# Performance work log

Hardware: AMD Instinct MI355X
Metric: run time of the kernel (lower is better)

The kernel has to match this reference:

```python
import jax, jax.numpy as jnp
import numpy as np

N, E = 20000, 640000
F_IN, H, T = 64, 256, 64  # in_channels = T, edge_attr dim = T -> EdgeConv MLP in = 3*T


def _lin(key, fan_in, fan_out):
    k1, k2 = jax.random.split(key)
    s = 1.0 / np.sqrt(fan_in)
    W = jax.random.uniform(k1, (fan_in, fan_out), jnp.float32, -s, s)
    b = jax.random.uniform(k2, (fan_out,), jnp.float32, -s, s)
    return W, b


def setup_inputs() -> dict:
    key = jax.random.key(0)
    ks = jax.random.split(key, 12)
    x = jax.random.normal(ks[0], (N, F_IN), jnp.float32)
    edge_index = jax.random.randint(ks[1], (2, E), 0, N, jnp.int32)
    edge_attr = jax.random.normal(ks[2], (E, T), jnp.float32)
    conv1_W, conv1_b = _lin(ks[3], F_IN, H)
    e_W1, e_b1 = _lin(ks[4], 3 * T, H)
    e_W2, e_b2 = _lin(ks[5], H, H)
    conv2_W, conv2_b = _lin(ks[6], 2 * H, H)
    conv3_W, conv3_b = _lin(ks[7], H, F_IN)
    lin1_W, lin1_b = _lin(ks[8], 2 * F_IN, F_IN)
    lin2_W, lin2_b = _lin(ks[9], F_IN, 128)
    lin3_W, lin3_b = _lin(ks[10], 128, 32)
    lin4_W, lin4_b = _lin(ks[11], 32, 2)
    return dict(x=x, edge_index=edge_index, edge_attr=edge_attr,
                conv1_W=conv1_W, conv1_b=conv1_b,
                e_W1=e_W1, e_b1=e_b1, e_W2=e_W2, e_b2=e_b2,
                conv2_W=conv2_W, conv2_b=conv2_b,
                conv3_W=conv3_W, conv3_b=conv3_b,
                lin1_W=lin1_W, lin1_b=lin1_b, lin2_W=lin2_W, lin2_b=lin2_b,
                lin3_W=lin3_W, lin3_b=lin3_b, lin4_W=lin4_W, lin4_b=lin4_b)


def reference(x, edge_index, edge_attr,
              conv1_W, conv1_b, e_W1, e_b1, e_W2, e_b2,
              conv2_W, conv2_b, conv3_W, conv3_b,
              lin1_W, lin1_b, lin2_W, lin2_b, lin3_W, lin3_b, lin4_W, lin4_b):
    n = x.shape[0]
    src, dst = edge_index[0], edge_index[1]
    # GCN symmetric norm with self-loops (deg counted on dst, +1 for self-loop)
    deg = jax.ops.segment_sum(jnp.ones_like(src, jnp.float32), dst, num_segments=n) + 1.0
    dis = jax.lax.rsqrt(deg)

    def gcn(h, W, b):
        hw = h @ W
        msg = hw[src] * (dis[src] * dis[dst])[:, None]
        # self-loop contribution: norm = dis[i]^2
        return jax.ops.segment_sum(msg, dst, num_segments=n) + hw * (dis * dis)[:, None] + b

    out1 = jax.nn.relu(gcn(x, conv1_W, conv1_b))
    # EdgeConv: MLP(cat[x_i, x_j, edge_attr]) with max aggregation onto dst (x_i = target)
    m = jnp.concatenate([x[dst], x[src], edge_attr], axis=1)      # [E, 3T]
    m = jax.nn.relu(m @ e_W1 + e_b1) @ e_W2 + e_b2                 # [E, H]
    agg = jax.ops.segment_max(m, dst, num_segments=n)
    agg = jnp.where(jnp.isfinite(agg), agg, 0.0)                   # nodes with no in-edges
    out_e1 = jax.nn.relu(agg)

    out2 = jax.nn.relu(gcn(jnp.concatenate([out1, out_e1], axis=1), conv2_W, conv2_b))
    out3 = jax.nn.relu(gcn(out2, conv3_W, conv3_b))
    h = jnp.concatenate([x, out3], axis=1)
    h = jax.nn.softplus(h @ lin1_W + lin1_b)
    h = jax.nn.softplus(h @ lin2_W + lin2_b)
    h = jax.nn.softplus(h @ lin3_W + lin3_b)
    h = h @ lin4_W + lin4_b                                        # [N, 2]
    return (h[:, 0], h[:, 1])
```

## Files before the change

### kernel.cpp

```cpp
#include <hip/hip_runtime.h>
#include <stdint.h>

typedef __bf16 bf16x8 __attribute__((ext_vector_type(8)));
typedef float f32x4 __attribute__((ext_vector_type(4)));
typedef unsigned short u16x8 __attribute__((ext_vector_type(8)));
typedef unsigned long long ull_t;
typedef unsigned short ushort_t;

#define DEV __device__ __forceinline__

DEV unsigned short f2bf(float f) {
  __bf16 b = (__bf16)f;
  return __builtin_bit_cast(unsigned short, b);
}

DEV float bf2f(unsigned short b) { return __uint_as_float((unsigned int)b << 16); }

DEV f32x4 zero4() { f32x4 z = {0.f, 0.f, 0.f, 0.f}; return z; }

DEV float softplusf(float v) { return (v > 15.f) ? v : log1pf(expf(v)); }

__global__ void pack_weight(const float* __restrict__ W, unsigned short* __restrict__ P,
                            int K, int Ncols) {
  int idx = blockIdx.x * 256 + threadIdx.x;
  if (idx >= K * Ncols) return;
  int j = idx & 7;
  int lane = (idx >> 3) & 63;
  int rest = idx >> 9;
  int NT = Ncols >> 4;
  int nt = rest % NT;
  int kt = rest / NT;
  int k = kt * 32 + ((j >> 2) * 16) + ((lane >> 4) * 4) + (j & 3);
  int col = nt * 16 + (lane & 15);
  P[idx] = f2bf(W[(size_t)k * Ncols + col]);
}

__global__ void k_deg(const int* __restrict__ dst, int* __restrict__ degi, int E) {
  int i = blockIdx.x * 256 + threadIdx.x;
  if (i < E) atomicAdd(&degi[dst[i]], 1);
}

__global__ void k_dis(const int* __restrict__ degi, float* __restrict__ dis, int n) {
  int i = blockIdx.x * 256 + threadIdx.x;
  if (i < n) dis[i] = rsqrtf((float)degi[i] + 1.0f);
}

__global__ __launch_bounds__(1024) void k_scan(const int* __restrict__ degi,
                                               int* __restrict__ ptr, int n) {
  __shared__ int part[1024];
  const int tid = threadIdx.x;
  const int chunk = (n + 1023) / 1024;
  const int b = tid * chunk;
  const int e2 = min(n, b + chunk);
  int s = 0;
  for (int i = b; i < e2; ++i) s += degi[i];
  part[tid] = s;
  __syncthreads();
  for (int off = 1; off < 1024; off <<= 1) {
    int val = (tid >= off) ? part[tid - off] : 0;
    __syncthreads();
    part[tid] += val;
    __syncthreads();
  }
  int run = (tid == 0) ? 0 : part[tid - 1];
  for (int i = b; i < e2; ++i) {
    ptr[i] = run;
    run += degi[i];
  }
  if (tid == 1023) ptr[n] = run;
}

__global__ void k_fill(const int* __restrict__ srcs, const int* __restrict__ dsts,
                       const int* __restrict__ ptr, const float* __restrict__ dis,
                       int* __restrict__ fillc,
                       int2* __restrict__ sc_s, int* __restrict__ dst_s,
                       int* __restrict__ perm_s, int E) {
  int e = blockIdx.x * 256 + threadIdx.x;
  if (e >= E) return;
  int d = dsts[e];
  int s = srcs[e];
  int pos = ptr[d] + atomicAdd(&fillc[d], 1);
  float c = dis[s] * dis[d];
  sc_s[pos] = make_int2(s, __float_as_int(c));
  dst_s[pos] = d;
  perm_s[pos] = e;
}

template <int COLS, bool FINALIZE, bool INBF16>
__global__ __launch_bounds__(256) void k_gather_agg(
    const void* __restrict__ featv, const int2* __restrict__ sc,
    const int* __restrict__ ptr, const float* __restrict__ dis,
    const void* __restrict__ hwv, const float* __restrict__ bias,
    float* __restrict__ out, int n) {
  constexpr int V = COLS / 64;
  const int v = blockIdx.x * 4 + (threadIdx.x >> 6);
  if (v >= n) return;
  const int lane = threadIdx.x & 63;
  const int beg = ptr[v], end = ptr[v + 1];

  auto loadrow = [&](int s, float* f) {
    if constexpr (INBF16) {
      const ushort_t* feat = (const ushort_t*)featv;
      if constexpr (V == 4) {
        ushort4 u = *(const ushort4*)(feat + (size_t)s * COLS + lane * 4);
        f[0] = bf2f(u.x); f[1] = bf2f(u.y); f[2] = bf2f(u.z); f[3] = bf2f(u.w);
      } else {
        f[0] = bf2f(feat[(size_t)s * COLS + lane]);
      }
    } else {
      const float* feat = (const float*)featv;
      if constexpr (V == 4) {
        float4 q = *(const float4*)(feat + (size_t)s * COLS + lane * 4);
        f[0] = q.x; f[1] = q.y; f[2] = q.z; f[3] = q.w;
      } else {
        f[0] = feat[(size_t)s * COLS + lane];
      }
    }
  };

  float acc[V];
#pragma unroll
  for (int i = 0; i < V; ++i) acc[i] = 0.f;
  const int cnt = end - beg;
  const int2* scp = sc + beg;
  int i = 0;
  for (; i + 4 <= cnt; i += 4) {
    int2 s0 = scp[i], s1 = scp[i + 1], s2 = scp[i + 2], s3 = scp[i + 3];
    float f0[V], f1[V], f2[V], f3[V];
    loadrow(s0.x, f0); loadrow(s1.x, f1); loadrow(s2.x, f2); loadrow(s3.x, f3);
    float c0 = __int_as_float(s0.y), c1 = __int_as_float(s1.y);
    float c2 = __int_as_float(s2.y), c3 = __int_as_float(s3.y);
#pragma unroll
    for (int j = 0; j < V; ++j)
      acc[j] += f0[j] * c0 + f1[j] * c1 + f2[j] * c2 + f3[j] * c3;
  }
  for (; i < cnt; ++i) {
    int2 s0 = scp[i];
    float c0 = __int_as_float(s0.y);
    float f0[V];
    loadrow(s0.x, f0);
#pragma unroll
    for (int j = 0; j < V; ++j) acc[j] += f0[j] * c0;
  }
  float* op = out + (size_t)v * COLS + lane * V;
  if constexpr (FINALIZE) {
    const float dv = dis[v];
    float d2 = dv * dv;
    float h[V];
    if constexpr (INBF16) {
      const ushort_t* hw = (const ushort_t*)hwv;
      if constexpr (V == 4) {
        ushort4 u = *(const ushort4*)(hw + (size_t)v * COLS + lane * 4);
        h[0] = bf2f(u.x); h[1] = bf2f(u.y); h[2] = bf2f(u.z); h[3] = bf2f(u.w);
      } else {
        h[0] = bf2f(hw[(size_t)v * COLS + lane]);
      }
    } else {
      const float* hw = (const float*)hwv;
      if constexpr (V == 4) {
        float4 q = *(const float4*)(hw + (size_t)v * COLS + lane * 4);
        h[0] = q.x; h[1] = q.y; h[2] = q.z; h[3] = q.w;
      } else {
        h[0] = hw[(size_t)v * COLS + lane];
      }
    }
#pragma unroll
    for (int i2 = 0; i2 < V; ++i2)
      acc[i2] = fmaxf(acc[i2] + h[i2] * d2 + bias[lane * V + i2], 0.f);
  }
  if constexpr (V == 4) {
    *(float4*)op = make_float4(acc[0], acc[1], acc[2], acc[3]);
  } else {
    op[0] = acc[0];
  }
}

template <int K, int NOUT, bool COMPOSE, bool RELUBIAS, bool OUTBF16>
__global__ __launch_bounds__(256, 2) void gcn_gemm(
    const float* __restrict__ inA, const float* __restrict__ inB,
    const float* __restrict__ dis,
    const unsigned short* __restrict__ Wp, const float* __restrict__ bias,
    void* __restrict__ outv, int out_stride, int nrows) {
  constexpr int NT = NOUT / 16;
  constexpr int NTW = NOUT / 64;
  __shared__ unsigned short s_in[64 * K];
  const int tid = threadIdx.x;
  const int r0 = blockIdx.x * 64;

  constexpr int C4R = K / 4;
  for (int idx = tid; idx < 64 * C4R; idx += 256) {
    int row = idx / C4R;
    int rem = idx - row * C4R;
    int grow = r0 + row;
    float4 v = make_float4(0.f, 0.f, 0.f, 0.f);
    if (grow < nrows) {
      v = *(const float4*)&inA[(size_t)grow * K + rem * 4];
      if constexpr (COMPOSE) {
        float d = dis[grow];
        d *= d;
        float4 w2 = *(const float4*)&inB[(size_t)grow * K + rem * 4];
        v.x += w2.x * d; v.y += w2.y * d; v.z += w2.z * d; v.w += w2.w * d;
      }
    }
    ushort4 b;
    b.x = f2bf(v.x); b.y = f2bf(v.y); b.z = f2bf(v.z); b.w = f2bf(v.w);
    *(ushort4*)&s_in[row * K + ((rem ^ (row & 7)) * 4)] = b;
  }
  __syncthreads();

  const int lane = tid & 63, wid = tid >> 6;
  const int lr = lane & 15, lg = lane >> 4;
  f32x4 acc[4][NTW];
#pragma unroll
  for (int m = 0; m < 4; ++m)
#pragma unroll
    for (int n2 = 0; n2 < NTW; ++n2) acc[m][n2] = zero4();

#pragma unroll
  for (int kt = 0; kt < K / 32; ++kt) {
    bf16x8 a[4];
#pragma unroll
    for (int m = 0; m < 4; ++m) {
      int rA = m * 16 + lr;
      int c1 = (kt * 8 + lg) ^ (rA & 7);
      int c2 = (kt * 8 + lg + 4) ^ (rA & 7);
      union { bf16x8 v; ull_t q[2]; } u;
      u.q[0] = *(const ull_t*)&s_in[rA * K + c1 * 4];
      u.q[1] = *(const ull_t*)&s_in[rA * K + c2 * 4];
      a[m] = u.v;
    }
#pragma unroll
    for (int n2 = 0; n2 < NTW; ++n2) {
      int nt = wid * NTW + n2;
      bf16x8 b = *(const bf16x8*)&Wp[(((kt * NT + nt) * 64 + lane) * 8)];
#pragma unroll
      for (int m = 0; m < 4; ++m)
        acc[m][n2] = __builtin_amdgcn_mfma_f32_16x16x32_bf16(a[m], b, acc[m][n2], 0, 0, 0);
    }
  }

#pragma unroll
  for (int n2 = 0; n2 < NTW; ++n2) {
    int col = (wid * NTW + n2) * 16 + lr;
    float bv = 0.f;
    if (RELUBIAS) bv = bias[col];
#pragma unroll
    for (int m = 0; m < 4; ++m) {
#pragma unroll
      for (int r = 0; r < 4; ++r) {
        int grow = r0 + m * 16 + lg * 4 + r;
        if (grow < nrows) {
          float v = acc[m][n2][r];
          if (RELUBIAS) v = fmaxf(v + bv, 0.f);
          if constexpr (OUTBF16) {
            ((ushort_t*)outv)[(size_t)grow * out_stride + col] = f2bf(v);
          } else {
            ((float*)outv)[(size_t)grow * out_stride + col] = v;
          }
        }
      }
    }
  }
}

__global__ __launch_bounds__(512, 4) void k_edgeconv(
    const float* __restrict__ x, const float* __restrict__ ea,
    const int2* __restrict__ sc_s, const int* __restrict__ dst_s,
    const int* __restrict__ perm_s,
    const unsigned short* __restrict__ W1p, const float* __restrict__ b1,
    const unsigned short* __restrict__ W2p, const float* __restrict__ b2,
    float* __restrict__ h2, int E) {
  __shared__ unsigned short s_buf[256 * 72];
  __shared__ int s_src[64], s_dst[64], s_perm[64];
  __shared__ ull_t s_mask;
  const int tid = threadIdx.x;
  const int e0 = blockIdx.x * 64;
  const int lane = tid & 63, wid = tid >> 6;
  if (tid < 64) {
    int e = e0 + tid;
    s_src[tid] = (e < E) ? sc_s[e].x : 0;
    s_dst[tid] = (e < E) ? dst_s[e] : 0;
    s_perm[tid] = (e < E) ? perm_s[e] : 0;
  }
  __syncthreads();
  if (wid == 0) {
    bool chg = (lane > 0) && (s_dst[lane] != s_dst[lane - 1]);
    ull_t m = __ballot(chg);
    if (lane == 0) s_mask = m;
  }
#pragma unroll
  for (int seg = 0; seg < 3; ++seg) {
#pragma unroll
    for (int it = 0; it < 2; ++it) {
      int idx = it * 512 + tid;
      int ei = idx >> 4;
      int q = idx & 15;
      const float* row;
      if (seg == 0) row = x + (unsigned)s_dst[ei] * 64u;
      else if (seg == 1) row = x + (unsigned)s_src[ei] * 64u;
      else row = ea + (unsigned)s_perm[ei] * 64u;
      float4 v = make_float4(0.f, 0.f, 0.f, 0.f);
      if (e0 + ei < E) v = *(const float4*)(row + q * 4);
      ushort4 b;
      b.x = f2bf(v.x); b.y = f2bf(v.y); b.z = f2bf(v.z); b.w = f2bf(v.w);
      int chunk = (seg * 16 + q) ^ (ei & 7);
      *(ushort4*)&s_buf[ei * 192 + chunk * 4] = b;
    }
  }
  __syncthreads();

  const int wr = wid >> 2;
  const int wc = wid & 3;
  const int lr = lane & 15, lg = lane >> 4;
  f32x4 acc[2][4];
#pragma unroll
  for (int m = 0; m < 2; ++m)
#pragma unroll
    for (int n2 = 0; n2 < 4; ++n2) acc[m][n2] = zero4();

#pragma unroll
  for (int kt = 0; kt < 6; ++kt) {
    bf16x8 a[2];
#pragma unroll
    for (int m = 0; m < 2; ++m) {
      int rA = wr * 32 + m * 16 + lr;
      int rr = rA & 7;
      union { bf16x8 v; ull_t q[2]; } u;
      u.q[0] = *(const ull_t*)&s_buf[rA * 192 + ((kt * 8 + lg) ^ rr) * 4];
      u.q[1] = *(const ull_t*)&s_buf[rA * 192 + ((kt * 8 + lg + 4) ^ rr) * 4];
      a[m] = u.v;
    }
#pragma unroll
    for (int n2 = 0; n2 < 4; ++n2) {
      int nt = wc * 4 + n2;
      int boff = ((kt * 16 + nt) * 64 + lane) * 8;
      bf16x8 b = *(const bf16x8*)&W1p[boff];
#pragma unroll
      for (int m = 0; m < 2; ++m)
        acc[m][n2] = __builtin_amdgcn_mfma_f32_16x16x32_bf16(a[m], b, acc[m][n2], 0, 0, 0);
    }
  }
  __syncthreads();

#pragma unroll
  for (int n2 = 0; n2 < 4; ++n2) {
    int col = (wc * 4 + n2) * 16 + lr;
    float bv = b1[col];
    int chunk0 = col >> 2, cm = col & 3;
#pragma unroll
    for (int m = 0; m < 2; ++m)
#pragma unroll
      for (int r = 0; r < 4; ++r) {
        int row = wr * 32 + m * 16 + lg * 4 + r;
        float v = fmaxf(acc[m][n2][r] + bv, 0.f);
        s_buf[row * 256 + ((chunk0 ^ (row & 7)) * 4) + cm] = f2bf(v);
      }
  }
  __syncthreads();

#pragma unroll
  for (int m = 0; m < 2; ++m)
#pragma unroll
    for (int n2 = 0; n2 < 4; ++n2) acc[m][n2] = zero4();
#pragma unroll
  for (int kt = 0; kt < 8; ++kt) {
    bf16x8 a[2];
#pragma unroll
    for (int m = 0; m < 2; ++m) {
      int rA = wr * 32 + m * 16 + lr;
      int rr = rA & 7;
      union { bf16x8 v; ull_t q[2]; } u;
      u.q[0] = *(const ull_t*)&s_buf[rA * 256 + ((kt * 8 + lg) ^ rr) * 4];
      u.q[1] = *(const ull_t*)&s_buf[rA * 256 + ((kt * 8 + lg + 4) ^ rr) * 4];
      a[m] = u.v;
    }
#pragma unroll
    for (int n2 = 0; n2 < 4; ++n2) {
      int nt = wc * 4 + n2;
      int boff = ((kt * 16 + nt) * 64 + lane) * 8;
      bf16x8 b = *(const bf16x8*)&W2p[boff];
#pragma unroll
      for (int m = 0; m < 2; ++m)
        acc[m][n2] = __builtin_amdgcn_mfma_f32_16x16x32_bf16(a[m], b, acc[m][n2], 0, 0, 0);
    }
  }
  __syncthreads();

#pragma unroll
  for (int n2 = 0; n2 < 4; ++n2) {
    int col = (wc * 4 + n2) * 16 + lr;
    float bv = b2[col];
#pragma unroll
    for (int m = 0; m < 2; ++m) {
      int rbase = wr * 32 + m * 16 + lg * 4;
      union { ushort_t h[4]; ull_t q; } pk;
#pragma unroll
      for (int r = 0; r < 4; ++r) {
        int row = rbase + r;
        float v = (e0 + row < E) ? fmaxf(acc[m][n2][r] + bv, 0.f) : 0.f;
        pk.h[r] = f2bf(v);
      }
      *(ull_t*)&s_buf[col * 72 + rbase] = pk.q;
    }
  }
  __syncthreads();

  {
    const int col = tid & 255;
    const int half = tid >> 8;
    const int rbeg = half * 32;
    const unsigned int mask = (unsigned int)(s_mask >> rbeg);
    unsigned int run = 0;
    int segstart = rbeg;
#pragma unroll
    for (int i = 0; i < 4; ++i) {
      u16x8 pack = *(const u16x8*)&s_buf[col * 72 + rbeg + i * 8];
#pragma unroll
      for (int r2 = 0; r2 < 8; ++r2) {
        int rloc = i * 8 + r2;
        if (mask & (1u << rloc)) {
          if (run > 0)
            atomicMax((int*)h2 + ((unsigned)s_dst[segstart] * 512u + 256u + col),
                      (int)(run << 16));
          run = 0;
          segstart = rbeg + rloc;
        }
        run = max(run, (unsigned int)pack[r2]);
      }
    }
    if (run > 0)
      atomicMax((int*)h2 + ((unsigned)s_dst[segstart] * 512u + 256u + col),
                (int)(run << 16));
  }
}

__global__ __launch_bounds__(256) void k_head(
    const float* __restrict__ x, const float* __restrict__ out3,
    const float* __restrict__ W1, const float* __restrict__ b1,
    const float* __restrict__ W2, const float* __restrict__ b2,
    const float* __restrict__ W3, const float* __restrict__ b3,
    const float* __restrict__ W4, const float* __restrict__ b4,
    float* __restrict__ out, int n) {
  __shared__ float sW1[128 * 64];
  __shared__ float sW3[128 * 32];
  __shared__ float sW4[32 * 2];
  __shared__ float sb1[64], sb2[128], sb3[32], sb4[2];
  __shared__ float sbuf[4][352];
  const int tid = threadIdx.x;
  for (int i = tid; i < 128 * 64; i += 256) sW1[i] = W1[i];
  for (int i = tid; i < 128 * 32; i += 256) sW3[i] = W3[i];
  if (tid < 64) sW4[tid] = W4[tid];
  if (tid < 64) sb1[tid] = b1[tid];
  if (tid < 128) sb2[tid] = b2[tid];
  if (tid < 32) sb3[tid] = b3[tid];
  if (tid < 2) sb4[tid] = b4[tid];
  __syncthreads();
  const int wid = tid >> 6, lane = tid & 63;
  float* B = sbuf[wid];
  const int per = gridDim.x * 4;
  const int iters = (n + per - 1) / per;
  for (int it = 0; it < iters; ++it) {
    const int node = it * per + blockIdx.x * 4 + wid;
    const bool act = node < n;
    if (act) {
      B[lane] = x[(size_t)node * 64 + lane];
      B[64 + lane] = out3[(size_t)node * 64 + lane];
    }
    __syncthreads();
    if (act) {
      float o = sb1[lane];
#pragma unroll 8
      for (int k = 0; k < 128; ++k) o += B[k] * sW1[k * 64 + lane];
      B[128 + lane] = softplusf(o);
    }
    __syncthreads();
    if (act) {
      float o0 = sb2[lane], o1 = sb2[64 + lane];
#pragma unroll 8
      for (int k = 0; k < 64; ++k) {
        float v = B[128 + k];
        o0 += v * W2[k * 128 + lane];
        o1 += v * W2[k * 128 + 64 + lane];
      }
      B[192 + lane] = softplusf(o0);
      B[256 + lane] = softplusf(o1);
    }
    __syncthreads();
    if (act && lane < 32) {
      float o = sb3[lane];
#pragma unroll 8
      for (int k = 0; k < 128; ++k) o += B[192 + k] * sW3[k * 32 + lane];
      B[320 + lane] = softplusf(o);
    }
    __syncthreads();
    if (act && lane < 2) {
      float o = sb4[lane];
#pragma unroll
      for (int k = 0; k < 32; ++k) o += B[320 + k] * sW4[k * 2 + lane];
      out[(size_t)lane * n + node] = o;
    }
    __syncthreads();
  }
}

static inline size_t alignup(size_t v) { return (v + 255) & ~(size_t)255; }

extern "C" void kernel_launch(void* const* d_in, const int* in_sizes, int n_in,
                              void* d_out, int out_size, void* d_ws, size_t ws_size,
                              hipStream_t stream) {
  const float* x = (const float*)d_in[0];
  const int* ei = (const int*)d_in[1];
  const float* ea = (const float*)d_in[2];
  const float* c1W = (const float*)d_in[3];
  const float* c1b = (const float*)d_in[4];
  const float* eW1 = (const float*)d_in[5];
  const float* eb1 = (const float*)d_in[6];
  const float* eW2 = (const float*)d_in[7];
  const float* eb2 = (const float*)d_in[8];
  const float* c2W = (const float*)d_in[9];
  const float* c2b = (const float*)d_in[10];
  const float* c3W = (const float*)d_in[11];
  const float* c3b = (const float*)d_in[12];
  const float* l1W = (const float*)d_in[13];
  const float* l1b = (const float*)d_in[14];
  const float* l2W = (const float*)d_in[15];
  const float* l2b = (const float*)d_in[16];
  const float* l3W = (const float*)d_in[17];
  const float* l3b = (const float*)d_in[18];
  const float* l4W = (const float*)d_in[19];
  const float* l4b = (const float*)d_in[20];
  const int n = in_sizes[0] / 64;
  const int E = in_sizes[1] / 2;
  const int* srcs = ei;
  const int* dsts = ei + E;

  char* w = (char*)d_ws;
  auto alloc = [&](size_t bytes) {
    char* p = w;
    w += alignup(bytes);
    return p;
  };
  float* dis = (float*)alloc((size_t)n * 4);
  int* degi = (int*)alloc((size_t)n * 4);
  int* ptr = (int*)alloc((size_t)(n + 1) * 4);
  int* fillc = (int*)alloc((size_t)n * 4);
  int2* sc_s = (int2*)alloc((size_t)E * 8);
  int* dst_s = (int*)alloc((size_t)E * 4);
  int* perm_s = (int*)alloc((size_t)E * 4);
  float* agg1 = (float*)alloc((size_t)n * 64 * 4);
  float* h2 = (float*)alloc((size_t)n * 512 * 4);
  ushort_t* hw2b = (ushort_t*)alloc((size_t)n * 256 * 2);
  float* out2 = (float*)alloc((size_t)n * 256 * 4);
  ushort_t* hw3b = (ushort_t*)alloc((size_t)n * 64 * 2);
  float* out3 = (float*)alloc((size_t)n * 64 * 4);
  unsigned short* p_c1 = (unsigned short*)alloc(64 * 256 * 2);
  unsigned short* p_e1 = (unsigned short*)alloc(192 * 256 * 2);
  unsigned short* p_e2 = (unsigned short*)alloc(256 * 256 * 2);
  unsigned short* p_c2 = (unsigned short*)alloc(512 * 256 * 2);
  unsigned short* p_c3 = (unsigned short*)alloc(256 * 64 * 2);

  hipMemsetAsync(degi, 0, (size_t)n * 4, stream);
  hipMemsetAsync(fillc, 0, (size_t)n * 4, stream);
  hipMemsetAsync(h2, 0, (size_t)n * 512 * 4, stream);

  pack_weight<<<(64 * 256) / 256, 256, 0, stream>>>(c1W, p_c1, 64, 256);
  pack_weight<<<(192 * 256) / 256, 256, 0, stream>>>(eW1, p_e1, 192, 256);
  pack_weight<<<(256 * 256) / 256, 256, 0, stream>>>(eW2, p_e2, 256, 256);
  pack_weight<<<(512 * 256) / 256, 256, 0, stream>>>(c2W, p_c2, 512, 256);
  pack_weight<<<(256 * 64) / 256, 256, 0, stream>>>(c3W, p_c3, 256, 64);

  k_deg<<<(E + 255) / 256, 256, 0, stream>>>(dsts, degi, E);
  k_dis<<<(n + 255) / 256, 256, 0, stream>>>(degi, dis, n);
  k_scan<<<1, 1024, 0, stream>>>(degi, ptr, n);
  k_fill<<<(E + 255) / 256, 256, 0, stream>>>(srcs, dsts, ptr, dis, fillc,
                                              sc_s, dst_s, perm_s, E);

  const int ablocks = (n + 3) / 4;
  const int gblocks = (n + 63) / 64;

  k_gather_agg<64, false, false><<<ablocks, 256, 0, stream>>>(
      x, sc_s, ptr, dis, nullptr, nullptr, agg1, n);
  gcn_gemm<64, 256, true, true, false><<<gblocks, 256, 0, stream>>>(
      agg1, x, dis, p_c1, c1b, h2, 512, n);

  k_edgeconv<<<(E + 63) / 64, 512, 0, stream>>>(x, ea, sc_s, dst_s, perm_s,
                                                p_e1, eb1, p_e2, eb2, h2, E);

  gcn_gemm<512, 256, false, false, true><<<gblocks, 256, 0, stream>>>(
      h2, nullptr, nullptr, p_c2, nullptr, hw2b, 256, n);
  k_gather_agg<256, true, true><<<ablocks, 256, 0, stream>>>(
      hw2b, sc_s, ptr, dis, hw2b, c2b, out2, n);

  gcn_gemm<256, 64, false, false, true><<<gblocks, 256, 0, stream>>>(
      out2, nullptr, nullptr, p_c3, nullptr, hw3b, 64, n);
  k_gather_agg<64, true, true><<<ablocks, 256, 0, stream>>>(
      hw3b, sc_s, ptr, dis, hw3b, c3b, out3, n);

  k_head<<<1250, 256, 0, stream>>>(x, out3, l1W, l1b, l2W, l2b, l3W, l3b, l4W, l4b,
                                   (float*)d_out, n);
}
```

Before: 610.6 us.

## Precompute per-node x_dst projection for EdgeConv first layer and gather bf16 x

The x[dst] slice of the EdgeConv first-layer GEMM is hoisted into a per-node GEMM (x @ W1a + b1) computed once for 20k nodes instead of 640k edges. Each edge then adds that row back via a permuted-column gather, using a matching k-permutation of the second-layer weights so the store is a packed 4-element write. x is also pre-converted to bf16 so the src gather reads half the bytes, and the per-edge K shrinks from 192 to 128. The cost is an extra n×256 fp32 buffer that every edge must read from global memory.

```diff
diff --git a/kernel.cpp b/kernel.cpp
--- a/kernel.cpp
+++ b/kernel.cpp
@@ -21,7 +21,7 @@
 DEV float softplusf(float v) { return (v > 15.f) ? v : log1pf(expf(v)); }
 
 __global__ void pack_weight(const float* __restrict__ W, unsigned short* __restrict__ P,
-                            int K, int Ncols) {
+                            int K, int Ncols, int permk) {
   int idx = blockIdx.x * 256 + threadIdx.x;
   if (idx >= K * Ncols) return;
   int j = idx & 7;
@@ -31,8 +31,19 @@
   int nt = rest % NT;
   int kt = rest / NT;
   int k = kt * 32 + ((j >> 2) * 16) + ((lane >> 4) * 4) + (j & 3);
+  if (permk) k = (k & ~63) | ((k & 3) << 4) | ((k >> 2) & 15);
   int col = nt * 16 + (lane & 15);
   P[idx] = f2bf(W[(size_t)k * Ncols + col]);
+}
+
+__global__ void k_cvt_bf16(const float* __restrict__ in, ushort_t* __restrict__ out,
+                           int n4) {
+  int i = blockIdx.x * 256 + threadIdx.x;
+  if (i >= n4) return;
+  float4 v = *(const float4*)(in + (size_t)i * 4);
+  ushort4 b;
+  b.x = f2bf(v.x); b.y = f2bf(v.y); b.z = f2bf(v.z); b.w = f2bf(v.w);
+  *(ushort4*)(out + (size_t)i * 4) = b;
 }
 
 __global__ void k_deg(const int* __restrict__ dst, int* __restrict__ degi, int E) {
@@ -175,7 +186,8 @@
   }
 }
 
-template <int K, int NOUT, bool COMPOSE, bool RELUBIAS, bool OUTBF16>
+template <int K, int NOUT, bool COMPOSE, bool RELUBIAS, bool OUTBF16,
+          bool ADDBIAS, bool PERMOUT>
 __global__ __launch_bounds__(256, 2) void gcn_gemm(
     const float* __restrict__ inA, const float* __restrict__ inB,
     const float* __restrict__ dis,
@@ -243,7 +255,9 @@
   for (int n2 = 0; n2 < NTW; ++n2) {
     int col = (wid * NTW + n2) * 16 + lr;
     float bv = 0.f;
-    if (RELUBIAS) bv = bias[col];
+    if (RELUBIAS || ADDBIAS) bv = bias[col];
+    int colw = col;
+    if (PERMOUT) colw = (col & ~63) | ((col & 15) << 2) | ((col >> 4) & 3);
 #pragma unroll
     for (int m = 0; m < 4; ++m) {
 #pragma unroll
@@ -252,10 +266,11 @@
         if (grow < nrows) {
           float v = acc[m][n2][r];
           if (RELUBIAS) v = fmaxf(v + bv, 0.f);
+          else if (ADDBIAS) v = v + bv;
           if constexpr (OUTBF16) {
-            ((ushort_t*)outv)[(size_t)grow * out_stride + col] = f2bf(v);
+            ((ushort_t*)outv)[(size_t)grow * out_stride + colw] = f2bf(v);
           } else {
-            ((float*)outv)[(size_t)grow * out_stride + col] = v;
+            ((float*)outv)[(size_t)grow * out_stride + colw] = v;
           }
         }
       }
@@ -264,10 +279,10 @@
 }
 
 __global__ __launch_bounds__(512, 4) void k_edgeconv(
-    const float* __restrict__ x, const float* __restrict__ ea,
+    const ushort_t* __restrict__ xb, const float* __restrict__ ea,
     const int2* __restrict__ sc_s, const int* __restrict__ dst_s,
     const int* __restrict__ perm_s,
-    const unsigned short* __restrict__ W1p, const float* __restrict__ b1,
+    const unsigned short* __restrict__ W1p, const float* __restrict__ h1p,
     const unsigned short* __restrict__ W2p, const float* __restrict__ b2,
     float* __restrict__ h2, int E) {
   __shared__ unsigned short s_buf[256 * 72];
@@ -289,22 +304,23 @@
     if (lane == 0) s_mask = m;
   }
 #pragma unroll
-  for (int seg = 0; seg < 3; ++seg) {
+  for (int seg = 0; seg < 2; ++seg) {
 #pragma unroll
     for (int it = 0; it < 2; ++it) {
       int idx = it * 512 + tid;
       int ei = idx >> 4;
       int q = idx & 15;
-      const float* row;
-      if (seg == 0) row = x + (unsigned)s_dst[ei] * 64u;
-      else if (seg == 1) row = x + (unsigned)s_src[ei] * 64u;
-      else row = ea + (unsigned)s_perm[ei] * 64u;
-      float4 v = make_float4(0.f, 0.f, 0.f, 0.f);
-      if (e0 + ei < E) v = *(const float4*)(row + q * 4);
       ushort4 b;
-      b.x = f2bf(v.x); b.y = f2bf(v.y); b.z = f2bf(v.z); b.w = f2bf(v.w);
+      if (seg == 0) {
+        b = *(const ushort4*)(xb + (unsigned)s_src[ei] * 64u + q * 4);
+      } else {
+        const float* row = ea + (unsigned)s_perm[ei] * 64u;
+        float4 v = make_float4(0.f, 0.f, 0.f, 0.f);
+        if (e0 + ei < E) v = *(const float4*)(row + q * 4);
+        b.x = f2bf(v.x); b.y = f2bf(v.y); b.z = f2bf(v.z); b.w = f2bf(v.w);
+      }
       int chunk = (seg * 16 + q) ^ (ei & 7);
-      *(ushort4*)&s_buf[ei * 192 + chunk * 4] = b;
+      *(ushort4*)&s_buf[ei * 128 + chunk * 4] = b;
     }
   }
   __syncthreads();
@@ -319,15 +335,15 @@
     for (int n2 = 0; n2 < 4; ++n2) acc[m][n2] = zero4();
 
 #pragma unroll
-  for (int kt = 0; kt < 6; ++kt) {
+  for (int kt = 0; kt < 4; ++kt) {
     bf16x8 a[2];
 #pragma unroll
     for (int m = 0; m < 2; ++m) {
       int rA = wr * 32 + m * 16 + lr;
       int rr = rA & 7;
       union { bf16x8 v; ull_t q[2]; } u;
-      u.q[0] = *(const ull_t*)&s_buf[rA * 192 + ((kt * 8 + lg) ^ rr) * 4];
-      u.q[1] = *(const ull_t*)&s_buf[rA * 192 + ((kt * 8 + lg + 4) ^ rr) * 4];
+      u.q[0] = *(const ull_t*)&s_buf[rA * 128 + ((kt * 8 + lg) ^ rr) * 4];
+      u.q[1] = *(const ull_t*)&s_buf[rA * 128 + ((kt * 8 + lg + 4) ^ rr) * 4];
       a[m] = u.v;
     }
 #pragma unroll
@@ -343,18 +359,20 @@
   __syncthreads();
 
 #pragma unroll
-  for (int n2 = 0; n2 < 4; ++n2) {
-    int col = (wc * 4 + n2) * 16 + lr;
-    float bv = b1[col];
-    int chunk0 = col >> 2, cm = col & 3;
-#pragma unroll
-    for (int m = 0; m < 2; ++m)
-#pragma unroll
-      for (int r = 0; r < 4; ++r) {
-        int row = wr * 32 + m * 16 + lg * 4 + r;
-        float v = fmaxf(acc[m][n2][r] + bv, 0.f);
-        s_buf[row * 256 + ((chunk0 ^ (row & 7)) * 4) + cm] = f2bf(v);
-      }
+  for (int m = 0; m < 2; ++m) {
+#pragma unroll
+    for (int r = 0; r < 4; ++r) {
+      int row = wr * 32 + m * 16 + lg * 4 + r;
+      float4 hq = *(const float4*)(h1p + (size_t)(unsigned)s_dst[row] * 256u +
+                                   wc * 64 + lr * 4);
+      union { ushort_t h[4]; ull_t q; } pk;
+      pk.h[0] = f2bf(fmaxf(acc[0][0][r] * 0.f + acc[m][0][r] + hq.x, 0.f));
+      pk.h[1] = f2bf(fmaxf(acc[m][1][r] + hq.y, 0.f));
+      pk.h[2] = f2bf(fmaxf(acc[m][2][r] + hq.z, 0.f));
+      pk.h[3] = f2bf(fmaxf(acc[m][3][r] + hq.w, 0.f));
+      int chunk = (wc * 16 + lr) ^ (row & 7);
+      *(ull_t*)&s_buf[row * 256 + chunk * 4] = pk.q;
+    }
   }
   __syncthreads();
 
@@ -553,8 +571,11 @@
   float* out2 = (float*)alloc((size_t)n * 256 * 4);
   ushort_t* hw3b = (ushort_t*)alloc((size_t)n * 64 * 2);
   float* out3 = (float*)alloc((size_t)n * 64 * 4);
+  ushort_t* xb = (ushort_t*)alloc((size_t)n * 64 * 2);
+  float* h1p = (float*)alloc((size_t)n * 256 * 4);
   unsigned short* p_c1 = (unsigned short*)alloc(64 * 256 * 2);
-  unsigned short* p_e1 = (unsigned short*)alloc(192 * 256 * 2);
+  unsigned short* p_e1a = (unsigned short*)alloc(64 * 256 * 2);
+  unsigned short* p_e1b = (unsigned short*)alloc(128 * 256 * 2);
   unsigned short* p_e2 = (unsigned short*)alloc(256 * 256 * 2);
   unsigned short* p_c2 = (unsigned short*)alloc(512 * 256 * 2);
   unsigned short* p_c3 = (unsigned short*)alloc(256 * 64 * 2);
@@ -563,11 +584,13 @@
   hipMemsetAsync(fillc, 0, (size_t)n * 4, stream);
   hipMemsetAsync(h2, 0, (size_t)n * 512 * 4, stream);
 
-  pack_weight<<<(64 * 256) / 256, 256, 0, stream>>>(c1W, p_c1, 64, 256);
-  pack_weight<<<(192 * 256) / 256, 256, 0, stream>>>(eW1, p_e1, 192, 256);
-  pack_weight<<<(256 * 256) / 256, 256, 0, stream>>>(eW2, p_e2, 256, 256);
-  pack_weight<<<(512 * 256) / 256, 256, 0, stream>>>(c2W, p_c2, 512, 256);
-  pack_weight<<<(256 * 64) / 256, 256, 0, stream>>>(c3W, p_c3, 256, 64);
+  pack_weight<<<(64 * 256) / 256, 256, 0, stream>>>(c1W, p_c1, 64, 256, 0);
+  pack_weight<<<(64 * 256) / 256, 256, 0, stream>>>(eW1, p_e1a, 64, 256, 0);
+  pack_weight<<<(128 * 256) / 256, 256, 0, stream>>>(eW1 + 64 * 256, p_e1b, 128, 256, 0);
+  pack_weight<<<(256 * 256) / 256, 256, 0, stream>>>(eW2, p_e2, 256, 256, 1);
+  pack_weight<<<(512 * 256) / 256, 256, 0, stream>>>(c2W, p_c2, 512, 256, 0);
+  pack_weight<<<(256 * 64) / 256, 256, 0, stream>>>(c3W, p_c3, 256, 64, 0);
+  k_cvt_bf16<<<(n * 16 + 255) / 256, 256, 0, stream>>>(x, xb, n * 16);
 
   k_deg<<<(E + 255) / 256, 256, 0, stream>>>(dsts, degi, E);
   k_dis<<<(n + 255) / 256, 256, 0, stream>>>(degi, dis, n);
@@ -578,20 +601,23 @@
   const int ablocks = (n + 3) / 4;
   const int gblocks = (n + 63) / 64;
 
+  gcn_gemm<64, 256, false, false, false, true, true><<<gblocks, 256, 0, stream>>>(
+      x, nullptr, nullptr, p_e1a, eb1, h1p, 256, n);
+
   k_gather_agg<64, false, false><<<ablocks, 256, 0, stream>>>(
       x, sc_s, ptr, dis, nullptr, nullptr, agg1, n);
-  gcn_gemm<64, 256, true, true, false><<<gblocks, 256, 0, stream>>>(
+  gcn_gemm<64, 256, true, true, false, false, false><<<gblocks, 256, 0, stream>>>(
       agg1, x, dis, p_c1, c1b, h2, 512, n);
 
-  k_edgeconv<<<(E + 63) / 64, 512, 0, stream>>>(x, ea, sc_s, dst_s, perm_s,
-                                                p_e1, eb1, p_e2, eb2, h2, E);
-
-  gcn_gemm<512, 256, false, false, true><<<gblocks, 256, 0, stream>>>(
+  k_edgeconv<<<(E + 63) / 64, 512, 0, stream>>>(xb, ea, sc_s, dst_s, perm_s,
+                                                p_e1b, h1p, p_e2, eb2, h2, E);
+
+  gcn_gemm<512, 256, false, false, true, false, false><<<gblocks, 256, 0, stream>>>(
       h2, nullptr, nullptr, p_c2, nullptr, hw2b, 256, n);
   k_gather_agg<256, true, true><<<ablocks, 256, 0, stream>>>(
       hw2b, sc_s, ptr, dis, hw2b, c2b, out2, n);
 
-  gcn_gemm<256, 64, false, false, true><<<gblocks, 256, 0, stream>>>(
+  gcn_gemm<256, 64, false, false, true, false, false><<<gblocks, 256, 0, stream>>>(
       out2, nullptr, nullptr, p_c3, nullptr, hw3b, 64, n);
   k_gather_agg<64, true, true><<<ablocks, 256, 0, stream>>>(
       hw3b, sc_s, ptr, dis, hw3b, c3b, out3, n);
```

New measurement: 617.0 us. Within noise of the previous version (+1.0%).

## Prefetch EdgeConv MLP weight fragments and pack hidden activations with permuted K

Applied to the files above, without the earlier changes.

The EdgeConv kernel now loads each k-step's W1/W2 MFMA B fragments one iteration ahead into registers, and issues the first loads before the barriers, so global-load latency overlaps the MFMAs. The hidden-layer epilogue writes four adjacent accumulator columns as one 64-bit LDS store instead of scalar 16-bit stores. This changes the K ordering of the intermediate tile, so the second-layer weights are packed with a matching K permutation. It costs more vector registers and could lower occupancy.

```diff
diff --git a/kernel.cpp b/kernel.cpp
--- a/kernel.cpp
+++ b/kernel.cpp
@@ -21,7 +21,7 @@
 DEV float softplusf(float v) { return (v > 15.f) ? v : log1pf(expf(v)); }
 
 __global__ void pack_weight(const float* __restrict__ W, unsigned short* __restrict__ P,
-                            int K, int Ncols) {
+                            int K, int Ncols, int permk) {
   int idx = blockIdx.x * 256 + threadIdx.x;
   if (idx >= K * Ncols) return;
   int j = idx & 7;
@@ -31,6 +31,7 @@
   int nt = rest % NT;
   int kt = rest / NT;
   int k = kt * 32 + ((j >> 2) * 16) + ((lane >> 4) * 4) + (j & 3);
+  if (permk) k = (k & ~63) | ((k & 3) << 4) | ((k >> 2) & 15);
   int col = nt * 16 + (lane & 15);
   P[idx] = f2bf(W[(size_t)k * Ncols + col]);
 }
@@ -307,11 +308,18 @@
       *(ushort4*)&s_buf[ei * 192 + chunk * 4] = b;
     }
   }
-  __syncthreads();
 
   const int wr = wid >> 2;
   const int wc = wid & 3;
   const int lr = lane & 15, lg = lane >> 4;
+
+  bf16x8 bn1[4];
+#pragma unroll
+  for (int n2 = 0; n2 < 4; ++n2)
+    bn1[n2] = *(const bf16x8*)&W1p[(((0 * 16 + wc * 4 + n2) * 64 + lane) * 8)];
+
+  __syncthreads();
+
   f32x4 acc[2][4];
 #pragma unroll
   for (int m = 0; m < 2; ++m)
@@ -320,6 +328,14 @@
 
 #pragma unroll
   for (int kt = 0; kt < 6; ++kt) {
+    bf16x8 bc[4];
+#pragma unroll
+    for (int n2 = 0; n2 < 4; ++n2) bc[n2] = bn1[n2];
+    if (kt < 5) {
+#pragma unroll
+      for (int n2 = 0; n2 < 4; ++n2)
+        bn1[n2] = *(const bf16x8*)&W1p[((((kt + 1) * 16 + wc * 4 + n2) * 64 + lane) * 8)];
+    }
     bf16x8 a[2];
 #pragma unroll
     for (int m = 0; m < 2; ++m) {
@@ -331,30 +347,37 @@
       a[m] = u.v;
     }
 #pragma unroll
-    for (int n2 = 0; n2 < 4; ++n2) {
-      int nt = wc * 4 + n2;
-      int boff = ((kt * 16 + nt) * 64 + lane) * 8;
-      bf16x8 b = *(const bf16x8*)&W1p[boff];
+    for (int n2 = 0; n2 < 4; ++n2)
 #pragma unroll
       for (int m = 0; m < 2; ++m)
-        acc[m][n2] = __builtin_amdgcn_mfma_f32_16x16x32_bf16(a[m], b, acc[m][n2], 0, 0, 0);
-    }
-  }
-  __syncthreads();
-
-#pragma unroll
-  for (int n2 = 0; n2 < 4; ++n2) {
-    int col = (wc * 4 + n2) * 16 + lr;
-    float bv = b1[col];
-    int chunk0 = col >> 2, cm = col & 3;
-#pragma unroll
-    for (int m = 0; m < 2; ++m)
+        acc[m][n2] = __builtin_amdgcn_mfma_f32_16x16x32_bf16(a[m], bc[n2], acc[m][n2], 0, 0, 0);
+  }
+
+  bf16x8 bn2[4];
+#pragma unroll
+  for (int n2 = 0; n2 < 4; ++n2)
+    bn2[n2] = *(const bf16x8*)&W2p[(((0 * 16 + wc * 4 + n2) * 64 + lane) * 8)];
+
+  __syncthreads();
+
+  {
+    float b1v[4];
+#pragma unroll
+    for (int n2 = 0; n2 < 4; ++n2) b1v[n2] = b1[(wc * 4 + n2) * 16 + lr];
+#pragma unroll
+    for (int m = 0; m < 2; ++m) {
 #pragma unroll
       for (int r = 0; r < 4; ++r) {
         int row = wr * 32 + m * 16 + lg * 4 + r;
-        float v = fmaxf(acc[m][n2][r] + bv, 0.f);
-        s_buf[row * 256 + ((chunk0 ^ (row & 7)) * 4) + cm] = f2bf(v);
-      }
+        union { ushort_t h[4]; ull_t q; } pk;
+        pk.h[0] = f2bf(fmaxf(acc[m][0][r] + b1v[0], 0.f));
+        pk.h[1] = f2bf(fmaxf(acc[m][1][r] + b1v[1], 0.f));
+        pk.h[2] = f2bf(fmaxf(acc[m][2][r] + b1v[2], 0.f));
+        pk.h[3] = f2bf(fmaxf(acc[m][3][r] + b1v[3], 0.f));
+        int chunk = (wc * 16 + lr) ^ (row & 7);
+        *(ull_t*)&s_buf[row * 256 + chunk * 4] = pk.q;
+      }
+    }
   }
   __syncthreads();
 
@@ -364,6 +387,14 @@
     for (int n2 = 0; n2 < 4; ++n2) acc[m][n2] = zero4();
 #pragma unroll
   for (int kt = 0; kt < 8; ++kt) {
+    bf16x8 bc[4];
+#pragma unroll
+    for (int n2 = 0; n2 < 4; ++n2) bc[n2] = bn2[n2];
+    if (kt < 7) {
+#pragma unroll
+      for (int n2 = 0; n2 < 4; ++n2)
+        bn2[n2] = *(const bf16x8*)&W2p[((((kt + 1) * 16 + wc * 4 + n2) * 64 + lane) * 8)];
+    }
     bf16x8 a[2];
 #pragma unroll
     for (int m = 0; m < 2; ++m) {
@@ -375,14 +406,10 @@
       a[m] = u.v;
     }
 #pragma unroll
-    for (int n2 = 0; n2 < 4; ++n2) {
-      int nt = wc * 4 + n2;
-      int boff = ((kt * 16 + nt) * 64 + lane) * 8;
-      bf16x8 b = *(const bf16x8*)&W2p[boff];
+    for (int n2 = 0; n2 < 4; ++n2)
 #pragma unroll
       for (int m = 0; m < 2; ++m)
-        acc[m][n2] = __builtin_amdgcn_mfma_f32_16x16x32_bf16(a[m], b, acc[m][n2], 0, 0, 0);
-    }
+        acc[m][n2] = __builtin_amdgcn_mfma_f32_16x16x32_bf16(a[m], bc[n2], acc[m][n2], 0, 0, 0);
   }
   __syncthreads();
 
@@ -563,11 +590,11 @@
   hipMemsetAsync(fillc, 0, (size_t)n * 4, stream);
   hipMemsetAsync(h2, 0, (size_t)n * 512 * 4, stream);
 
-  pack_weight<<<(64 * 256) / 256, 256, 0, stream>>>(c1W, p_c1, 64, 256);
-  pack_weight<<<(192 * 256) / 256, 256, 0, stream>>>(eW1, p_e1, 192, 256);
-  pack_weight<<<(256 * 256) / 256, 256, 0, stream>>>(eW2, p_e2, 256, 256);
-  pack_weight<<<(512 * 256) / 256, 256, 0, stream>>>(c2W, p_c2, 512, 256);
-  pack_weight<<<(256 * 64) / 256, 256, 0, stream>>>(c3W, p_c3, 256, 64);
+  pack_weight<<<(64 * 256) / 256, 256, 0, stream>>>(c1W, p_c1, 64, 256, 0);
+  pack_weight<<<(192 * 256) / 256, 256, 0, stream>>>(eW1, p_e1, 192, 256, 0);
+  pack_weight<<<(256 * 256) / 256, 256, 0, stream>>>(eW2, p_e2, 256, 256, 1);
+  pack_weight<<<(512 * 256) / 256, 256, 0, stream>>>(c2W, p_c2, 512, 256, 0);
+  pack_weight<<<(256 * 64) / 256, 256, 0, stream>>>(c3W, p_c3, 256, 64, 0);
 
   k_deg<<<(E + 255) / 256, 256, 0, stream>>>(dsts, degi, E);
   k_dis<<<(n + 255) / 256, 256, 0, stream>>>(degi, dis, n);
```

Result: no change. 599.5 us (-1.8%).
